# Performance work log

Hardware: AMD Instinct MI355X
Metric: run time of the kernel (lower is better)

The kernel has to match this reference:

```python
import jax, jax.numpy as jnp
import numpy as np

# e2m1 (nvfp4) representable magnitudes and rounding midpoints
E2M1_POS = jnp.array([0.0, 0.5, 1.0, 1.5, 2.0, 3.0, 4.0, 6.0], dtype=jnp.float32)
E2M1_BOUNDS = jnp.array([0.25, 0.75, 1.25, 1.75, 2.5, 3.5, 5.0], dtype=jnp.float32)
E2M1_TABLE = jnp.concatenate([E2M1_POS, -E2M1_POS])  # 4-bit code -> value (sign bit = bit 3)
BLOCK = 16  # nvfp4 block-scale group size


def _fp8_round(v):
    # simulate storage of block scales in float8 e4m3
    return v.astype(jnp.float8_e4m3fn).astype(jnp.float32)


def _e2m1_round(v):
    # round-to-nearest onto the e2m1 grid (|v| must be pre-clipped to <= 6)
    idx = jnp.searchsorted(E2M1_BOUNDS, jnp.abs(v))
    return jnp.sign(v) * E2M1_POS[idx]


def setup_inputs() -> dict:
    key = jax.random.key(0)
    k1, k2, k3, k4, k5 = jax.random.split(key, 5)
    M, H = 4096, 4096
    x = jax.random.normal(k1, (M, 2 * H), dtype=jnp.float32)
    w = jax.random.randint(k2, (H, H // 2), 0, 256, dtype=jnp.int32)  # packed fp4, 2 nibbles/byte
    wscale = jax.random.normal(k3, (H, H // BLOCK), dtype=jnp.float32)  # cast to fp8 inside
    wscale2 = jax.random.uniform(k4, (1,), dtype=jnp.float32)
    scale = jax.random.uniform(k5, (1,), dtype=jnp.float32)
    return {"x": x, "w": w, "wscale": wscale, "wscale2": wscale2, "scale": scale}


def reference(x, w, wscale, wscale2, scale):
    M = x.shape[0]
    H = x.shape[1] // 2
    # SiLU-and-mul
    y = jax.nn.silu(x[:, :H]) * x[:, H:]                 # [M, H]
    gs = 1.0 / scale[0]                                  # global input scale (1/self.scale)
    # NVFP4 dynamic quant: per-16-element block amax -> fp8 block scale, values -> e2m1
    yb = y.reshape(M, H // BLOCK, BLOCK)
    amax = jnp.max(jnp.abs(yb), axis=-1)                 # [M, H/16]
    sf = _fp8_round(amax * (gs / 6.0))                   # fp8-stored block scales
    inv = jnp.where(sf > 0, gs / sf, 0.0)
    q = _e2m1_round(jnp.clip(yb * inv[..., None], -6.0, 6.0))
    a_deq = (q * sf[..., None]).reshape(M, H)            # fp4 value * fp8 block scale
    # Weight side: unpack fp4 nibbles (low nibble = even k), dequant with fp8 block scales
    wu = w.astype(jnp.uint8)
    lo = (wu & 0xF).astype(jnp.int32)
    hi = (wu >> 4).astype(jnp.int32)
    codes = jnp.stack([lo, hi], axis=-1).reshape(H, H)   # [N, K]
    b_q = E2M1_TABLE[codes]
    ws = _fp8_round(wscale)                              # model stores wscale in fp8
    b_deq = b_q * jnp.repeat(ws, BLOCK, axis=1)          # [N, K]
    # cutlass_scaled_fp4_mm with alpha = scale * wscale2 undoing global scales
    alpha = scale[0] * wscale2[0]
    out = alpha * (a_deq @ b_deq.T)                      # [M, N]
    return out
```

## Files before the change

### kernel.cpp

```cpp
#include <hip/hip_runtime.h>
#include <math.h>

typedef unsigned int uint;
typedef unsigned short ushort;
typedef __attribute__((ext_vector_type(8))) short bf16x8;
typedef __attribute__((ext_vector_type(4))) float f32x4;

static constexpr int Mdim = 4096;
static constexpr int Ndim = 4096;
static constexpr int Kdim = 4096;
static constexpr int Hdim = 4096;


__device__ __forceinline__ float fp8_round(float v) {
  float a = fabsf(v);
  float q;
  if (a >= 0x1p-6f) {
    uint u = __float_as_uint(a);
    int e = (int)(u >> 23) - 127;
    float quant = __uint_as_float((uint)(e - 3 + 127) << 23);
    q = rintf(a / quant) * quant;
    q = fminf(q, 448.f);
  } else {
    q = rintf(a * 512.f) * 0x1p-9f;
  }
  return copysignf(q, v);
}

__device__ __forceinline__ float e2m1_round(float t) {
  float a = fabsf(t);
  float q;
  if (a <= 0.25f) q = 0.f;
  else if (a <= 0.75f) q = 0.5f;
  else if (a <= 1.25f) q = 1.f;
  else if (a <= 1.75f) q = 1.5f;
  else if (a <= 2.5f)  q = 2.f;
  else if (a <= 3.5f)  q = 3.f;
  else if (a <= 5.f)   q = 4.f;
  else                 q = 6.f;
  return copysignf(q, t);
}

__device__ __forceinline__ float e2m1_decode(uint c) {
  uint m = c & 7u;
  float v;
  if (m == 0u) v = 0.f;
  else if (m == 1u) v = 0.5f;
  else v = __uint_as_float(((126u + (m >> 1)) << 23) | ((m & 1u) << 22));
  return (c & 8u) ? -v : v;
}


__global__ void prep_kernel(const float* __restrict__ x, const int* __restrict__ w,
                            const float* __restrict__ wscale,
                            const float* __restrict__ scalep,
                            ushort* __restrict__ a_deq, ushort* __restrict__ b_deq) {
  const int b = blockIdx.x;
  if (b < Mdim) {
    const int row = b;
    const int blk = threadIdx.x;
    const float gs = 1.0f / scalep[0];
    const float c6 = gs / 6.0f;
    const float* gp = x + (size_t)row * (2 * Hdim) + blk * 16;
    const float* up = gp + Hdim;
    float y[16];
    float amax = 0.f;
#pragma unroll
    for (int i = 0; i < 4; ++i) {
      float4 gv = ((const float4*)gp)[i];
      float4 uv = ((const float4*)up)[i];
      float ga[4] = {gv.x, gv.y, gv.z, gv.w};
      float ua[4] = {uv.x, uv.y, uv.z, uv.w};
#pragma unroll
      for (int j = 0; j < 4; ++j) {
        float xv = ga[j];
        float sig = 1.0f / (1.0f + expf(-xv));
        float yy = xv * sig * ua[j];
        y[i * 4 + j] = yy;
        amax = fmaxf(amax, fabsf(yy));
      }
    }
    const float sf = fp8_round(amax * c6);
    uint outp[8];
    if (sf > 0.f) {
      const float inv = gs / sf;
#pragma unroll
      for (int i = 0; i < 8; ++i) {
        float t0 = fminf(fmaxf(y[2 * i] * inv, -6.f), 6.f);
        float t1 = fminf(fmaxf(y[2 * i + 1] * inv, -6.f), 6.f);
        float d0 = e2m1_round(t0) * sf;
        float d1 = e2m1_round(t1) * sf;
        outp[i] = (__float_as_uint(d0) >> 16) | ((__float_as_uint(d1) >> 16) << 16);
      }
    } else {
#pragma unroll
      for (int i = 0; i < 8; ++i) outp[i] = 0u;
    }
    uint4* dst = (uint4*)(a_deq + (size_t)row * Hdim + blk * 16);
    dst[0] = (uint4){outp[0], outp[1], outp[2], outp[3]};
    dst[1] = (uint4){outp[4], outp[5], outp[6], outp[7]};
  } else {
    const int n = b - Mdim;
    const int blk = threadIdx.x;
    const int4* wp = (const int4*)(w + (size_t)n * (Hdim / 2) + blk * 8);
    int4 w0 = wp[0], w1 = wp[1];
    int wb[8] = {w0.x, w0.y, w0.z, w0.w, w1.x, w1.y, w1.z, w1.w};
    const float ws = fp8_round(wscale[(size_t)n * (Hdim / 16) + blk]);
    uint outp[8];
#pragma unroll
    for (int i = 0; i < 8; ++i) {
      uint byte = (uint)wb[i] & 0xFFu;
      float vlo = e2m1_decode(byte & 15u) * ws;
      float vhi = e2m1_decode(byte >> 4) * ws;
      outp[i] = (__float_as_uint(vlo) >> 16) | ((__float_as_uint(vhi) >> 16) << 16);
    }
    uint4* dst = (uint4*)(b_deq + (size_t)n * Hdim + blk * 16);
    dst[0] = (uint4){outp[0], outp[1], outp[2], outp[3]};
    dst[1] = (uint4){outp[4], outp[5], outp[6], outp[7]};
  }
}


#define BM 256
#define BN 256
#define BK 64
#define NT (Kdim / BK)
#define TILE_E (256 * 64)

__device__ __forceinline__ void gload_lds16(const ushort* g, ushort* l) {
  __builtin_amdgcn_global_load_lds((const __attribute__((address_space(1))) void*)g,
                                   (__attribute__((address_space(3))) void*)l,
                                   16, 0, 0);
}

#define BAR()                                   \
  do {                                          \
    asm volatile("" ::: "memory");              \
    __builtin_amdgcn_s_barrier();               \
    asm volatile("" ::: "memory");              \
  } while (0)

__global__ __launch_bounds__(512, 2) void gemm256(const ushort* __restrict__ A,
                                                  const ushort* __restrict__ B,
                                                  float* __restrict__ C,
                                                  const float* __restrict__ scalep,
                                                  const float* __restrict__ wscale2p) {
  extern __shared__ __align__(16) ushort lds[];
  const int tid = threadIdx.x;
  const int wave = tid >> 6;
  const int lane = tid & 63;
  const int wm = wave >> 2;
  const int wn = wave & 3;
  const int fr = lane & 15;
  const int fq = lane >> 4;

  const int wg = blockIdx.x;
  const int swz = (wg & 7) * 32 + (wg >> 3);
  const int m0 = (swz >> 4) * BM;
  const int n0 = (swz & 15) * BN;

  f32x4 acc[8][4];
#pragma unroll
  for (int i = 0; i < 8; ++i)
#pragma unroll
    for (int j = 0; j < 4; ++j) acc[i][j] = (f32x4){0.f, 0.f, 0.f, 0.f};

  ushort* pA0 = lds;
  ushort* pA1 = lds + TILE_E;
  ushort* pA2 = lds + 2 * TILE_E;
  ushort* pB0 = lds + 3 * TILE_E;
  ushort* pB1 = lds + 4 * TILE_E;

  int goffA[4], goffB[4], loff[4];
#pragma unroll
  for (int h = 0; h < 2; ++h)
#pragma unroll
    for (int rr = 0; rr < 2; ++rr) {
      const int idx = h * 2 + rr;
      const int rowb = h * 128 + rr * 64 + wave * 8;
      const int trow = rowb + (lane >> 3);
      const int sc = (lane & 7) ^ (trow & 7);
      goffA[idx] = (m0 + trow) * Kdim + sc * 8;
      goffB[idx] = (n0 + trow) * Kdim + sc * 8;
      loff[idx] = rowb * 64;
    }

#define STAGE_A(h, kcol)                                                  \
  do {                                                                    \
    gload_lds16(A + (size_t)goffA[(h)*2 + 0] + (kcol), pA2 + loff[(h)*2 + 0]); \
    gload_lds16(A + (size_t)goffA[(h)*2 + 1] + (kcol), pA2 + loff[(h)*2 + 1]); \
  } while (0)
#define STAGE_B(h, kcol)                                                  \
  do {                                                                    \
    gload_lds16(B + (size_t)goffB[(h)*2 + 0] + (kcol), pB0 + loff[(h)*2 + 0]); \
    gload_lds16(B + (size_t)goffB[(h)*2 + 1] + (kcol), pB0 + loff[(h)*2 + 1]); \
  } while (0)

  const int laneAOff = (wm * 128 + fr) * 64;
  const int laneBOff = (wn * 64 + fr) * 64;
  const int xo0 = (fq ^ (fr & 7)) * 8;
  const int xo1 = ((4 + fq) ^ (fr & 7)) * 8;

  {
    ushort* sv = pA2;
    pA2 = pA0; STAGE_A(0, 0); STAGE_A(1, 0);
    STAGE_B(0, 0); STAGE_B(1, 0);
    pA2 = pA1; STAGE_A(0, BK); STAGE_A(1, BK);
    { ushort* t = pB0; pB0 = pB1; STAGE_B(0, BK); STAGE_B(1, BK); pB0 = t; }
    pA2 = sv;
  }
  asm volatile("s_waitcnt vmcnt(8)" ::: "memory");
  BAR();

  bf16x8 af0[2][2], bfr[4][2];
  {
    const ushort* aR0 = pA0 + laneAOff + xo0;
    const ushort* aR1 = pA0 + laneAOff + xo1;
    const ushort* bR0 = pB0 + laneBOff + xo0;
    const ushort* bR1 = pB0 + laneBOff + xo1;
#pragma unroll
    for (int ni = 0; ni < 4; ++ni) {
      bfr[ni][0] = *(const bf16x8*)(bR0 + ni * 1024);
      bfr[ni][1] = *(const bf16x8*)(bR1 + ni * 1024);
    }
#pragma unroll
    for (int m2 = 0; m2 < 2; ++m2) {
      af0[m2][0] = *(const bf16x8*)(aR0 + m2 * 1024);
      af0[m2][1] = *(const bf16x8*)(aR1 + m2 * 1024);
    }
  }

  for (int kt = 0; kt < NT; ++kt) {
    const int kc = (kt + 2) * BK;
    const bool stg = (kt + 2) < NT;
    const bool nxt = (kt + 1) < NT;
    const ushort* aR0 = pA0 + laneAOff + xo0;
    const ushort* aR1 = pA0 + laneAOff + xo1;
    bf16x8 af1[2][2], af2[2][2], af3[2][2];

#pragma unroll
    for (int m2 = 0; m2 < 2; ++m2) {
      af1[m2][0] = *(const bf16x8*)(aR0 + (2 + m2) * 1024);
      af1[m2][1] = *(const bf16x8*)(aR1 + (2 + m2) * 1024);
    }
    if (stg) STAGE_A(0, kc);
    BAR();
    __builtin_amdgcn_s_setprio(1);
#pragma unroll
    for (int m2 = 0; m2 < 2; ++m2)
#pragma unroll
      for (int ni = 0; ni < 4; ++ni)
#pragma unroll
        for (int kk = 0; kk < 2; ++kk)
          acc[m2][ni] = __builtin_amdgcn_mfma_f32_16x16x32_bf16(af0[m2][kk], bfr[ni][kk],
                                                                acc[m2][ni], 0, 0, 0);
    __builtin_amdgcn_s_setprio(0);
    BAR();

#pragma unroll
    for (int m2 = 0; m2 < 2; ++m2) {
      af2[m2][0] = *(const bf16x8*)(aR0 + (4 + m2) * 1024);
      af2[m2][1] = *(const bf16x8*)(aR1 + (4 + m2) * 1024);
    }
    if (stg) STAGE_A(1, kc);
    BAR();
    __builtin_amdgcn_s_setprio(1);
#pragma unroll
    for (int m2 = 0; m2 < 2; ++m2)
#pragma unroll
      for (int ni = 0; ni < 4; ++ni)
#pragma unroll
        for (int kk = 0; kk < 2; ++kk)
          acc[2 + m2][ni] = __builtin_amdgcn_mfma_f32_16x16x32_bf16(af1[m2][kk], bfr[ni][kk],
                                                                    acc[2 + m2][ni], 0, 0, 0);
    __builtin_amdgcn_s_setprio(0);
    BAR();

#pragma unroll
    for (int m2 = 0; m2 < 2; ++m2) {
      af3[m2][0] = *(const bf16x8*)(aR0 + (6 + m2) * 1024);
      af3[m2][1] = *(const bf16x8*)(aR1 + (6 + m2) * 1024);
    }
    if (stg) STAGE_B(0, kc);
    BAR();
    __builtin_amdgcn_s_setprio(1);
#pragma unroll
    for (int m2 = 0; m2 < 2; ++m2)
#pragma unroll
      for (int ni = 0; ni < 4; ++ni)
#pragma unroll
        for (int kk = 0; kk < 2; ++kk)
          acc[4 + m2][ni] = __builtin_amdgcn_mfma_f32_16x16x32_bf16(af2[m2][kk], bfr[ni][kk],
                                                                    acc[4 + m2][ni], 0, 0, 0);
    __builtin_amdgcn_s_setprio(0);
    if (stg) asm volatile("s_waitcnt vmcnt(6)" ::: "memory");
    else     asm volatile("s_waitcnt vmcnt(0)" ::: "memory");
    BAR();

    if (stg) STAGE_B(1, kc);
    BAR();
    __builtin_amdgcn_s_setprio(1);
#pragma unroll
    for (int m2 = 0; m2 < 2; ++m2)
#pragma unroll
      for (int ni = 0; ni < 4; ++ni)
#pragma unroll
        for (int kk = 0; kk < 2; ++kk)
          acc[6 + m2][ni] = __builtin_amdgcn_mfma_f32_16x16x32_bf16(af3[m2][kk], bfr[ni][kk],
                                                                    acc[6 + m2][ni], 0, 0, 0);
    __builtin_amdgcn_s_setprio(0);
    if (nxt) {
      const ushort* aN0 = pA1 + laneAOff + xo0;
      const ushort* aN1 = pA1 + laneAOff + xo1;
      const ushort* bN0 = pB1 + laneBOff + xo0;
      const ushort* bN1 = pB1 + laneBOff + xo1;
#pragma unroll
      for (int ni = 0; ni < 4; ++ni) {
        bfr[ni][0] = *(const bf16x8*)(bN0 + ni * 1024);
        bfr[ni][1] = *(const bf16x8*)(bN1 + ni * 1024);
      }
#pragma unroll
      for (int m2 = 0; m2 < 2; ++m2) {
        af0[m2][0] = *(const bf16x8*)(aN0 + m2 * 1024);
        af0[m2][1] = *(const bf16x8*)(aN1 + m2 * 1024);
      }
    }
    BAR();

    { ushort* t = pA0; pA0 = pA1; pA1 = pA2; pA2 = t; }
    { ushort* t = pB0; pB0 = pB1; pB1 = t; }
  }

  const float alpha = scalep[0] * wscale2p[0];
#pragma unroll
  for (int mi = 0; mi < 8; ++mi)
#pragma unroll
    for (int ni = 0; ni < 4; ++ni) {
      const int col = n0 + wn * 64 + ni * 16 + fr;
      const int rbase = m0 + wm * 128 + mi * 16 + fq * 4;
#pragma unroll
      for (int r = 0; r < 4; ++r)
        C[(size_t)(rbase + r) * Ndim + col] = alpha * acc[mi][ni][r];
    }
}


extern "C" void kernel_launch(void* const* d_in, const int* in_sizes, int n_in,
                              void* d_out, int out_size, void* d_ws, size_t ws_size,
                              hipStream_t stream) {
  const float* x       = (const float*)d_in[0];
  const int*   w       = (const int*)d_in[1];
  const float* wscale  = (const float*)d_in[2];
  const float* wscale2 = (const float*)d_in[3];
  const float* scale   = (const float*)d_in[4];
  float* out = (float*)d_out;

  ushort* a_deq = (ushort*)d_ws;
  ushort* b_deq = a_deq + (size_t)Mdim * Kdim;

  prep_kernel<<<Mdim + Ndim, 256, 0, stream>>>(x, w, wscale, scale, a_deq, b_deq);

  (void)hipFuncSetAttribute((const void*)gemm256, hipFuncAttributeMaxDynamicSharedMemorySize, 163840);
  gemm256<<<(Mdim / BM) * (Ndim / BN), 512, 163840, stream>>>(a_deq, b_deq, out, scale, wscale2);
}
```

Measured before the change: 158.0 us.

## Switch GEMM inner loop from 16x16x32 to 32x32x16 bf16 MFMA tiles

Replaces the 16x16x32 bf16 MFMA fragments with 32x32x16 MFMA, reorganizing the per-wave accumulators into 4x2 tiles of 16 floats and changing the LDS fragment read pattern and epilogue row mapping to match. The larger MFMA shape cuts LDS fragment reads per FLOP and the instruction count. The barrier placement is also restructured so each MFMA phase runs before its barrier instead of between two barriers, removing one barrier per phase. The risks are different LDS bank-conflict behaviour with the new swizzled reads and less interleaving slack.

```diff
diff --git a/kernel.cpp b/kernel.cpp
--- a/kernel.cpp
+++ b/kernel.cpp
@@ -4,7 +4,7 @@
 typedef unsigned int uint;
 typedef unsigned short ushort;
 typedef __attribute__((ext_vector_type(8))) short bf16x8;
-typedef __attribute__((ext_vector_type(4))) float f32x4;
+typedef __attribute__((ext_vector_type(16))) float f32x16;
 
 static constexpr int Mdim = 4096;
 static constexpr int Ndim = 4096;
@@ -151,19 +151,21 @@
   const int lane = tid & 63;
   const int wm = wave >> 2;
   const int wn = wave & 3;
-  const int fr = lane & 15;
-  const int fq = lane >> 4;
+  const int lr = lane & 31;
+  const int lh = lane >> 5;
 
   const int wg = blockIdx.x;
   const int swz = (wg & 7) * 32 + (wg >> 3);
   const int m0 = (swz >> 4) * BM;
   const int n0 = (swz & 15) * BN;
 
-  f32x4 acc[8][4];
-#pragma unroll
-  for (int i = 0; i < 8; ++i)
-#pragma unroll
-    for (int j = 0; j < 4; ++j) acc[i][j] = (f32x4){0.f, 0.f, 0.f, 0.f};
+  f32x16 acc[4][2];
+#pragma unroll
+  for (int mt = 0; mt < 4; ++mt)
+#pragma unroll
+    for (int nt = 0; nt < 2; ++nt)
+#pragma unroll
+      for (int r = 0; r < 16; ++r) acc[mt][nt][r] = 0.f;
 
   ushort* pA0 = lds;
   ushort* pA1 = lds + TILE_E;
@@ -185,21 +187,50 @@
       loff[idx] = rowb * 64;
     }
 
-#define STAGE_A(h, kcol)                                                  \
-  do {                                                                    \
+#define STAGE_A(h, kcol)                                                       \
+  do {                                                                         \
     gload_lds16(A + (size_t)goffA[(h)*2 + 0] + (kcol), pA2 + loff[(h)*2 + 0]); \
     gload_lds16(A + (size_t)goffA[(h)*2 + 1] + (kcol), pA2 + loff[(h)*2 + 1]); \
   } while (0)
-#define STAGE_B(h, kcol)                                                  \
-  do {                                                                    \
+#define STAGE_B(h, kcol)                                                       \
+  do {                                                                         \
     gload_lds16(B + (size_t)goffB[(h)*2 + 0] + (kcol), pB0 + loff[(h)*2 + 0]); \
     gload_lds16(B + (size_t)goffB[(h)*2 + 1] + (kcol), pB0 + loff[(h)*2 + 1]); \
   } while (0)
 
-  const int laneAOff = (wm * 128 + fr) * 64;
-  const int laneBOff = (wn * 64 + fr) * 64;
-  const int xo0 = (fq ^ (fr & 7)) * 8;
-  const int xo1 = ((4 + fq) ^ (fr & 7)) * 8;
+  const int laneA = (wm * 128 + lr) * 64;
+  const int laneB = (wn * 64 + lr) * 64;
+  int xk[4];
+#pragma unroll
+  for (int s = 0; s < 4; ++s) xk[s] = ((2 * s + lh) ^ (lr & 7)) * 8;
+
+#define RD_A(dst, base, mt)                                                \
+  do {                                                                     \
+    _Pragma("unroll")                                                      \
+    for (int s = 0; s < 4; ++s)                                            \
+      dst[s] = *(const bf16x8*)((base) + (mt) * 2048 + xk[s]);             \
+  } while (0)
+#define RD_B(dst, base)                                                    \
+  do {                                                                     \
+    _Pragma("unroll")                                                      \
+    for (int nt = 0; nt < 2; ++nt)                                         \
+      _Pragma("unroll")                                                    \
+      for (int s = 0; s < 4; ++s)                                          \
+        dst[nt][s] = *(const bf16x8*)((base) + nt * 2048 + xk[s]);         \
+  } while (0)
+
+#define MFMA_T(mt, AF)                                                         \
+  do {                                                                         \
+    __builtin_amdgcn_s_setprio(1);                                             \
+    _Pragma("unroll")                                                          \
+    for (int s = 0; s < 4; ++s) {                                              \
+      acc[mt][0] = __builtin_amdgcn_mfma_f32_32x32x16_bf16(AF[s], bfr[0][s],   \
+                                                           acc[mt][0], 0, 0, 0); \
+      acc[mt][1] = __builtin_amdgcn_mfma_f32_32x32x16_bf16(AF[s], bfr[1][s],   \
+                                                           acc[mt][1], 0, 0, 0); \
+    }                                                                          \
+    __builtin_amdgcn_s_setprio(0);                                             \
+  } while (0)
 
   {
     ushort* sv = pA2;
@@ -212,118 +243,38 @@
   asm volatile("s_waitcnt vmcnt(8)" ::: "memory");
   BAR();
 
-  bf16x8 af0[2][2], bfr[4][2];
-  {
-    const ushort* aR0 = pA0 + laneAOff + xo0;
-    const ushort* aR1 = pA0 + laneAOff + xo1;
-    const ushort* bR0 = pB0 + laneBOff + xo0;
-    const ushort* bR1 = pB0 + laneBOff + xo1;
-#pragma unroll
-    for (int ni = 0; ni < 4; ++ni) {
-      bfr[ni][0] = *(const bf16x8*)(bR0 + ni * 1024);
-      bfr[ni][1] = *(const bf16x8*)(bR1 + ni * 1024);
-    }
-#pragma unroll
-    for (int m2 = 0; m2 < 2; ++m2) {
-      af0[m2][0] = *(const bf16x8*)(aR0 + m2 * 1024);
-      af0[m2][1] = *(const bf16x8*)(aR1 + m2 * 1024);
-    }
-  }
+  bf16x8 af0[4], af1[4], af2[4], af3[4], bfr[2][4];
+  RD_A(af0, pA0 + laneA, 0);
+  RD_B(bfr, pB0 + laneB);
 
   for (int kt = 0; kt < NT; ++kt) {
     const int kc = (kt + 2) * BK;
     const bool stg = (kt + 2) < NT;
     const bool nxt = (kt + 1) < NT;
-    const ushort* aR0 = pA0 + laneAOff + xo0;
-    const ushort* aR1 = pA0 + laneAOff + xo1;
-    bf16x8 af1[2][2], af2[2][2], af3[2][2];
-
-#pragma unroll
-    for (int m2 = 0; m2 < 2; ++m2) {
-      af1[m2][0] = *(const bf16x8*)(aR0 + (2 + m2) * 1024);
-      af1[m2][1] = *(const bf16x8*)(aR1 + (2 + m2) * 1024);
-    }
+    const ushort* aB = pA0 + laneA;
+
+    RD_A(af1, aB, 1);
     if (stg) STAGE_A(0, kc);
+    MFMA_T(0, af0);
     BAR();
-    __builtin_amdgcn_s_setprio(1);
-#pragma unroll
-    for (int m2 = 0; m2 < 2; ++m2)
-#pragma unroll
-      for (int ni = 0; ni < 4; ++ni)
-#pragma unroll
-        for (int kk = 0; kk < 2; ++kk)
-          acc[m2][ni] = __builtin_amdgcn_mfma_f32_16x16x32_bf16(af0[m2][kk], bfr[ni][kk],
-                                                                acc[m2][ni], 0, 0, 0);
-    __builtin_amdgcn_s_setprio(0);
+
+    RD_A(af2, aB, 2);
+    if (stg) STAGE_A(1, kc);
+    MFMA_T(1, af1);
     BAR();
 
-#pragma unroll
-    for (int m2 = 0; m2 < 2; ++m2) {
-      af2[m2][0] = *(const bf16x8*)(aR0 + (4 + m2) * 1024);
-      af2[m2][1] = *(const bf16x8*)(aR1 + (4 + m2) * 1024);
-    }
-    if (stg) STAGE_A(1, kc);
-    BAR();
-    __builtin_amdgcn_s_setprio(1);
-#pragma unroll
-    for (int m2 = 0; m2 < 2; ++m2)
-#pragma unroll
-      for (int ni = 0; ni < 4; ++ni)
-#pragma unroll
-        for (int kk = 0; kk < 2; ++kk)
-          acc[2 + m2][ni] = __builtin_amdgcn_mfma_f32_16x16x32_bf16(af1[m2][kk], bfr[ni][kk],
-                                                                    acc[2 + m2][ni], 0, 0, 0);
-    __builtin_amdgcn_s_setprio(0);
-    BAR();
-
-#pragma unroll
-    for (int m2 = 0; m2 < 2; ++m2) {
-      af3[m2][0] = *(const bf16x8*)(aR0 + (6 + m2) * 1024);
-      af3[m2][1] = *(const bf16x8*)(aR1 + (6 + m2) * 1024);
-    }
+    RD_A(af3, aB, 3);
     if (stg) STAGE_B(0, kc);
-    BAR();
-    __builtin_amdgcn_s_setprio(1);
-#pragma unroll
-    for (int m2 = 0; m2 < 2; ++m2)
-#pragma unroll
-      for (int ni = 0; ni < 4; ++ni)
-#pragma unroll
-        for (int kk = 0; kk < 2; ++kk)
-          acc[4 + m2][ni] = __builtin_amdgcn_mfma_f32_16x16x32_bf16(af2[m2][kk], bfr[ni][kk],
-                                                                    acc[4 + m2][ni], 0, 0, 0);
-    __builtin_amdgcn_s_setprio(0);
+    MFMA_T(2, af2);
     if (stg) asm volatile("s_waitcnt vmcnt(6)" ::: "memory");
     else     asm volatile("s_waitcnt vmcnt(0)" ::: "memory");
     BAR();
 
     if (stg) STAGE_B(1, kc);
-    BAR();
-    __builtin_amdgcn_s_setprio(1);
-#pragma unroll
-    for (int m2 = 0; m2 < 2; ++m2)
-#pragma unroll
-      for (int ni = 0; ni < 4; ++ni)
-#pragma unroll
-        for (int kk = 0; kk < 2; ++kk)
-          acc[6 + m2][ni] = __builtin_amdgcn_mfma_f32_16x16x32_bf16(af3[m2][kk], bfr[ni][kk],
-                                                                    acc[6 + m2][ni], 0, 0, 0);
-    __builtin_amdgcn_s_setprio(0);
+    MFMA_T(3, af3);
     if (nxt) {
-      const ushort* aN0 = pA1 + laneAOff + xo0;
-      const ushort* aN1 = pA1 + laneAOff + xo1;
-      const ushort* bN0 = pB1 + laneBOff + xo0;
-      const ushort* bN1 = pB1 + laneBOff + xo1;
-#pragma unroll
-      for (int ni = 0; ni < 4; ++ni) {
-        bfr[ni][0] = *(const bf16x8*)(bN0 + ni * 1024);
-        bfr[ni][1] = *(const bf16x8*)(bN1 + ni * 1024);
-      }
-#pragma unroll
-      for (int m2 = 0; m2 < 2; ++m2) {
-        af0[m2][0] = *(const bf16x8*)(aN0 + m2 * 1024);
-        af0[m2][1] = *(const bf16x8*)(aN1 + m2 * 1024);
-      }
+      RD_A(af0, pA1 + laneA, 0);
+      RD_B(bfr, pB1 + laneB);
     }
     BAR();
 
@@ -333,14 +284,16 @@
 
   const float alpha = scalep[0] * wscale2p[0];
 #pragma unroll
-  for (int mi = 0; mi < 8; ++mi)
-#pragma unroll
-    for (int ni = 0; ni < 4; ++ni) {
-      const int col = n0 + wn * 64 + ni * 16 + fr;
-      const int rbase = m0 + wm * 128 + mi * 16 + fq * 4;
-#pragma unroll
-      for (int r = 0; r < 4; ++r)
-        C[(size_t)(rbase + r) * Ndim + col] = alpha * acc[mi][ni][r];
+  for (int mt = 0; mt < 4; ++mt)
+#pragma unroll
+    for (int nt = 0; nt < 2; ++nt) {
+      const int col = n0 + wn * 64 + nt * 32 + lr;
+      const int rbase = m0 + wm * 128 + mt * 32 + 4 * lh;
+#pragma unroll
+      for (int r = 0; r < 16; ++r) {
+        const int row = rbase + (r & 3) + 8 * (r >> 2);
+        C[(size_t)row * Ndim + col] = alpha * acc[mt][nt][r];
+      }
     }
 }
 
```

Result: slower. 169.3 us (+7.2%).
